# Kernel optimization log

Hardware: AMD Instinct MI355X
Metric: run time of the kernel (lower is better)

## Reference

```python
import jax, jax.numpy as jnp
import numpy as np

C, N, H = 1024, 64, 16
B, T = 4, 1024
DECAY_LORA, AAA_LORA, MV_LORA, GATE_LORA = 64, 64, 32, 128
EPS_GN = 0.00064


def setup_inputs() -> dict:
    key = jax.random.key(0)
    ks = iter(jax.random.split(key, 32))
    nrm = lambda shape, s=0.02: jax.random.normal(next(ks), shape, jnp.float32) * s
    uni = lambda shape: jax.random.uniform(next(ks), shape, jnp.float32)
    inp = {
        'x': jax.random.normal(next(ks), (B, T, C), jnp.float32),
        'x_r': uni((1, 1, C)), 'x_w': uni((1, 1, C)), 'x_k': uni((1, 1, C)),
        'x_v': uni((1, 1, C)), 'x_a': uni((1, 1, C)), 'x_g': uni((1, 1, C)),
        'w0': nrm((1, 1, C), 0.5), 'w1': nrm((C, DECAY_LORA)), 'w2': nrm((DECAY_LORA, C)),
        'a0': nrm((1, 1, C), 0.5), 'a1': nrm((C, AAA_LORA)), 'a2': nrm((AAA_LORA, C)),
        'v0': nrm((1, 1, C), 0.5), 'v1': nrm((C, MV_LORA)), 'v2': nrm((MV_LORA, C)),
        'g1': nrm((C, GATE_LORA)), 'g2': nrm((GATE_LORA, C)),
        'k_k': uni((1, 1, C)), 'k_a': uni((1, 1, C)), 'r_k': nrm((H, N), 0.1),
        'Wr': nrm((C, C)), 'Wk': nrm((C, C)), 'Wv': nrm((C, C)), 'Wo': nrm((C, C)),
        'ln_gamma': jnp.ones((C,), jnp.float32), 'ln_beta': jnp.zeros((C,), jnp.float32),
    }
    return inp


def rwkv7_op(r, w, k, v, a, b):
    # r,w,k,v,a,b: [B,T,C]; state S: [B,H,N,N] (rows=value dim, cols=key dim)
    Bb, Tt, Cc = r.shape
    to_t = lambda z: z.reshape(Bb, Tt, H, N).transpose(1, 0, 2, 3)  # [T,B,H,N]
    r_, k_, v_, a_, b_ = map(to_t, (r, k, v, a, b))
    w_ = jnp.exp(-jnp.exp(to_t(w)))  # decay in (0,1)
    def step(S, inp):
        rt, wt, kt, vt, at, bt = inp
        sa = jnp.einsum('bhij,bhj->bhi', S, at)                 # S @ a
        S = S * wt[:, :, None, :] + sa[..., None] * bt[:, :, None, :] \
            + vt[..., None] * kt[:, :, None, :]
        out = jnp.einsum('bhij,bhj->bhi', S, rt)
        return S, out
    S0 = jnp.zeros((Bb, H, N, N), r.dtype)
    _, outs = jax.lax.scan(step, S0, (r_, w_, k_, v_, a_, b_))
    return outs.transpose(1, 0, 2, 3).reshape(Bb, Tt, Cc)


def reference(x, x_r, x_w, x_k, x_v, x_a, x_g, w0, w1, w2, a0, a1, a2,
              v0, v1, v2, g1, g2, k_k, k_a, r_k, Wr, Wk, Wv, Wo,
              ln_gamma, ln_beta):
    Bb, Tt, Cc = x.shape
    # token shift
    xx = jnp.pad(x, ((0, 0), (1, 0), (0, 0)))[:, :-1] - x
    xr = x + xx * x_r; xw = x + xx * x_w; xk = x + xx * x_k
    xv = x + xx * x_v; xa = x + xx * x_a; xg = x + xx * x_g
    r = xr @ Wr
    w = -jax.nn.softplus(-(w0 + jnp.tanh(xw @ w1) @ w2)) - 0.5
    k = xk @ Wk
    v = xv @ Wv
    v_first = v  # first-layer case (v_first=None)
    a = jax.nn.sigmoid(a0 + xa @ a1 @ a2)
    g = jax.nn.sigmoid(xg @ g1) @ g2
    kk = k * k_k
    kkh = kk.reshape(Bb, Tt, H, N)
    kk = (kkh / jnp.maximum(jnp.linalg.norm(kkh, axis=-1, keepdims=True), 1e-12)).reshape(Bb, Tt, Cc)
    k = k * (1 + (a - 1) * k_a)
    o = rwkv7_op(r, w, k, v, -kk, kk * a)
    # group norm over H groups of N channels
    y = o.reshape(Bb * Tt, H, N)
    mu = jnp.mean(y, axis=-1, keepdims=True)
    var = jnp.var(y, axis=-1, keepdims=True)
    y = ((y - mu) * jax.lax.rsqrt(var + EPS_GN)).reshape(Bb, Tt, Cc) * ln_gamma + ln_beta
    rh = r.reshape(Bb, Tt, H, N)
    kh = k.reshape(Bb, Tt, H, N)
    vh = v.reshape(Bb, Tt, H, N)
    rwkv = jnp.sum(rh * kh * r_k, axis=-1, keepdims=True) * vh
    y = y + rwkv.reshape(Bb, Tt, Cc)
    out = (y * g) @ Wo
    return out, v_first
```

## Files before the change

### kernel.cpp

```cpp
#include <hip/hip_runtime.h>
#include <hip/hip_bf16.h>
#include <math.h>

#define BB 4
#define TT 1024
#define CCH 1024
#define HH 16
#define NNd 64
#define PAD 65
#define RS 72
#define LBS 68

typedef short bf16x8 __attribute__((ext_vector_type(8)));
typedef float f32x4 __attribute__((ext_vector_type(4)));

__device__ __forceinline__ unsigned short f2bf(float f) {
  __hip_bfloat16 h = __float2bfloat16(f);
  return __builtin_bit_cast(unsigned short, h);
}
__device__ __forceinline__ float bf2f(unsigned short u) {
  unsigned int x = (unsigned int)u << 16;
  return __builtin_bit_cast(float, x);
}
__device__ __forceinline__ float sigmoidf_(float x) {
  return __builtin_amdgcn_rcpf(1.0f + __expf(-x));
}
__device__ __forceinline__ float ftanh_(float x) {
  return 1.0f - 2.0f * __builtin_amdgcn_rcpf(__expf(2.0f * x) + 1.0f);
}

__device__ __forceinline__ void gl2lds16(const unsigned short* g, unsigned short* l) {
  __builtin_amdgcn_global_load_lds(
      (const __attribute__((address_space(1))) unsigned int*)g,
      (__attribute__((address_space(3))) unsigned int*)l, 16, 0, 0);
}

__device__ __forceinline__ void transpose_tile(
    const float* __restrict__ in, unsigned short* __restrict__ out,
    int R, int Cc, int r0, int c0, unsigned short (*tile)[68], int t)
{
  const int rr = t >> 4;
  const int cc = (t & 15) * 4;
#pragma unroll
  for (int p = 0; p < 4; ++p) {
    int row = p * 16 + rr;
    float4 v = *(const float4*)(in + (size_t)(r0 + row) * Cc + c0 + cc);
    tile[row][cc]     = f2bf(v.x);
    tile[row][cc + 1] = f2bf(v.y);
    tile[row][cc + 2] = f2bf(v.z);
    tile[row][cc + 3] = f2bf(v.w);
  }
  __syncthreads();
#pragma unroll
  for (int p = 0; p < 4; ++p) {
    int row = p * 16 + rr;
    ushort4 o;
    o.x = tile[cc][row];
    o.y = tile[cc + 1][row];
    o.z = tile[cc + 2][row];
    o.w = tile[cc + 3][row];
    *(ushort4*)(out + (size_t)(c0 + row) * R + r0 + cc) = o;
  }
}

__global__ __launch_bounds__(256) void prep_kernel(
    const float* __restrict__ x,
    const float* __restrict__ cr, const float* __restrict__ cw,
    const float* __restrict__ ck, const float* __restrict__ cv,
    const float* __restrict__ ca, const float* __restrict__ cg,
    unsigned short* __restrict__ xr, unsigned short* __restrict__ xw,
    unsigned short* __restrict__ xk, unsigned short* __restrict__ xv,
    unsigned short* __restrict__ xa, unsigned short* __restrict__ xg,
    const float* __restrict__ W0, const float* __restrict__ W1,
    const float* __restrict__ W2, const float* __restrict__ W3,
    unsigned short* __restrict__ T0, unsigned short* __restrict__ T1,
    unsigned short* __restrict__ T2, unsigned short* __restrict__ T3,
    const float* __restrict__ w1, const float* __restrict__ w2,
    const float* __restrict__ a1, const float* __restrict__ a2,
    const float* __restrict__ g1, const float* __restrict__ g2,
    unsigned short* __restrict__ w1T, unsigned short* __restrict__ w2T,
    unsigned short* __restrict__ a1T, unsigned short* __restrict__ a2T,
    unsigned short* __restrict__ g1T, unsigned short* __restrict__ g2T)
{
  __shared__ unsigned short tile[64][68];
  const int blk = blockIdx.x;
  const int tid = threadIdx.x;
  if (blk < 4096) {
    const size_t idx = ((size_t)blk * 256 + tid) * 4;
    const int c = (int)(idx & 1023);
    const int t = (int)((idx >> 10) & 1023);
    float4 xc = *(const float4*)(x + idx);
    float4 xp = make_float4(0.f, 0.f, 0.f, 0.f);
    if (t > 0) xp = *(const float4*)(x + idx - 1024);
    float4 dx = make_float4(xp.x - xc.x, xp.y - xc.y, xp.z - xc.z, xp.w - xc.w);
    auto st = [&](unsigned short* dst, const float* coef) {
      float4 w = *(const float4*)(coef + c);
      ushort4 o;
      o.x = f2bf(fmaf(dx.x, w.x, xc.x));
      o.y = f2bf(fmaf(dx.y, w.y, xc.y));
      o.z = f2bf(fmaf(dx.z, w.z, xc.z));
      o.w = f2bf(fmaf(dx.w, w.w, xc.w));
      *(ushort4*)(dst + idx) = o;
    };
    st(xr, cr); st(xw, cw); st(xk, ck); st(xv, cv); st(xa, ca); st(xg, cg);
  } else if (blk < 5120) {
    const int j = blk - 4096;
    const int z = j >> 8, rem = j & 255;
    const int ty = rem >> 4, tx = rem & 15;
    const float* src = (z == 0) ? W0 : (z == 1) ? W1 : (z == 2) ? W2 : W3;
    unsigned short* dst = (z == 0) ? T0 : (z == 1) ? T1 : (z == 2) ? T2 : T3;
    transpose_tile(src, dst, 1024, 1024, tx * 64, ty * 64, tile, tid);
  } else {
    const int i = blk - 5120;
    const float* src; unsigned short* dst; int R, C, rt, ct;
    if (i < 16)      { src = w1; dst = w1T; R = 1024; C = 64;   rt = i;      ct = 0; }
    else if (i < 32) { src = w2; dst = w2T; R = 64;   C = 1024; rt = 0;      ct = i - 16; }
    else if (i < 48) { src = a1; dst = a1T; R = 1024; C = 64;   rt = i - 32; ct = 0; }
    else if (i < 64) { src = a2; dst = a2T; R = 64;   C = 1024; rt = 0;      ct = i - 48; }
    else if (i < 96) { int k = i - 64; src = g1; dst = g1T; R = 1024; C = 128; rt = k >> 1; ct = k & 1; }
    else             { int k = i - 96; src = g2; dst = g2T; R = 128; C = 1024; rt = k & 1;  ct = k >> 1; }
    transpose_tile(src, dst, R, C, rt * 64, ct * 64, tile, tid);
  }
}

__global__ __launch_bounds__(256) void gemm_stage1_kernel(
    const unsigned short* __restrict__ xrB, const unsigned short* __restrict__ xkB,
    const unsigned short* __restrict__ xvB,
    const unsigned short* __restrict__ WrT, const unsigned short* __restrict__ WkT,
    const unsigned short* __restrict__ WvT,
    unsigned short* __restrict__ r_btc, unsigned short* __restrict__ k_btc,
    float* __restrict__ v_btc,
    const unsigned short* __restrict__ xwB, const unsigned short* __restrict__ xaB,
    const unsigned short* __restrict__ xgB,
    const unsigned short* __restrict__ w1T, const unsigned short* __restrict__ a1T,
    const unsigned short* __restrict__ g1T,
    unsigned short* __restrict__ hwB, unsigned short* __restrict__ haB,
    unsigned short* __restrict__ hgB)
{
  constexpr int K = 1024, SK = 32;
  __shared__ __align__(16) unsigned short As[128 * SK];
  __shared__ __align__(16) unsigned short Bs[128 * SK];
  const int blk = blockIdx.x;
  const int tid = threadIdx.x;
  const int wv = tid >> 6, lane = tid & 63;
  const int fr = lane & 15, q = lane >> 4;
  const int arow = tid >> 2;
  const int akc = (tid & 3) * 8;

  if (blk < 768) {
    const int z = blk >> 8, rem = blk & 255;
    const int m0 = (rem & 31) * 128;
    const int n0 = (rem >> 5) * 128;
    const unsigned short* A = (z == 0) ? xrB : (z == 1) ? xkB : xvB;
    const unsigned short* BT = (z == 0) ? WrT : (z == 1) ? WkT : WvT;
    const int wave_m = wv >> 1, wave_n = wv & 1;

    f32x4 acc[4][4];
#pragma unroll
    for (int i = 0; i < 4; i++)
#pragma unroll
      for (int j = 0; j < 4; j++) acc[i][j] = (f32x4){0.f, 0.f, 0.f, 0.f};

    for (int k0 = 0; k0 < K; k0 += 32) {
#pragma unroll
      for (int i = 0; i < 2; ++i)
        gl2lds16(A + (size_t)(m0 + arow + i * 64) * K + k0 + akc, As + i * 2048 + wv * 512);
#pragma unroll
      for (int i = 0; i < 2; ++i)
        gl2lds16(BT + (size_t)(n0 + arow + i * 64) * K + k0 + akc, Bs + i * 2048 + wv * 512);
      __syncthreads();
      bf16x8 af[4], bfv[4];
#pragma unroll
      for (int i = 0; i < 4; i++)
        af[i] = *(const bf16x8*)(&As[(wave_m * 64 + i * 16 + fr) * SK + q * 8]);
#pragma unroll
      for (int j = 0; j < 4; j++)
        bfv[j] = *(const bf16x8*)(&Bs[(wave_n * 64 + j * 16 + fr) * SK + q * 8]);
#pragma unroll
      for (int i = 0; i < 4; i++)
#pragma unroll
        for (int j = 0; j < 4; j++)
          acc[i][j] = __builtin_amdgcn_mfma_f32_16x16x32_bf16(af[i], bfv[j], acc[i][j], 0, 0, 0);
      __syncthreads();
    }
#pragma unroll
    for (int i = 0; i < 4; i++)
#pragma unroll
      for (int j = 0; j < 4; j++) {
        const int mb = m0 + wave_m * 64 + i * 16 + q * 4;
        const int n = n0 + wave_n * 64 + j * 16 + fr;
#pragma unroll
        for (int r = 0; r < 4; r++) {
          if (z == 0)      r_btc[(size_t)(mb + r) * 1024 + n] = f2bf(acc[i][j][r]);
          else if (z == 1) k_btc[(size_t)(mb + r) * 1024 + n] = f2bf(acc[i][j][r]);
          else             v_btc[(size_t)(mb + r) * 1024 + n] = acc[i][j][r];
        }
      }
  } else {
    const int j2 = blk - 768;
    const int y = j2 >> 5;
    const int m0 = (j2 & 31) * 128;
    const unsigned short* A  = (y == 0) ? xwB : (y == 1) ? xaB : xgB;
    const unsigned short* BT = (y == 0) ? w1T : (y == 1) ? a1T : (g1T + (size_t)(y - 2) * 64 * K);
    unsigned short* outb = (y == 0) ? hwB : (y == 1) ? haB : hgB;
    const int Nout = (y < 2) ? 64 : 128;
    const int ncol0 = (y < 2) ? 0 : (y - 2) * 64;

    f32x4 acc[2][4];
#pragma unroll
    for (int i = 0; i < 2; i++)
#pragma unroll
      for (int j = 0; j < 4; j++) acc[i][j] = (f32x4){0.f, 0.f, 0.f, 0.f};

    for (int k0 = 0; k0 < K; k0 += 32) {
#pragma unroll
      for (int i = 0; i < 2; ++i)
        gl2lds16(A + (size_t)(m0 + arow + i * 64) * K + k0 + akc, As + i * 2048 + wv * 512);
      gl2lds16(BT + (size_t)arow * K + k0 + akc, Bs + wv * 512);
      __syncthreads();
      bf16x8 af[2], bfv[4];
#pragma unroll
      for (int i = 0; i < 2; i++)
        af[i] = *(const bf16x8*)(&As[(wv * 32 + i * 16 + fr) * SK + q * 8]);
#pragma unroll
      for (int j = 0; j < 4; j++)
        bfv[j] = *(const bf16x8*)(&Bs[(j * 16 + fr) * SK + q * 8]);
#pragma unroll
      for (int i = 0; i < 2; i++)
#pragma unroll
        for (int j = 0; j < 4; j++)
          acc[i][j] = __builtin_amdgcn_mfma_f32_16x16x32_bf16(af[i], bfv[j], acc[i][j], 0, 0, 0);
      __syncthreads();
    }
#pragma unroll
    for (int i = 0; i < 2; i++)
#pragma unroll
      for (int j = 0; j < 4; j++) {
        const int mb = m0 + wv * 32 + i * 16 + q * 4;
        const int n = ncol0 + j * 16 + fr;
#pragma unroll
        for (int r = 0; r < 4; r++) {
          float val = acc[i][j][r];
          if (y == 0) val = ftanh_(val);
          else if (y >= 2) val = sigmoidf_(val);
          outb[(size_t)(mb + r) * Nout + n] = f2bf(val);
        }
      }
  }
}

__global__ __launch_bounds__(256) void lora2_kernel(
    const unsigned short* __restrict__ hwB, const unsigned short* __restrict__ haB,
    const unsigned short* __restrict__ hgB,
    const unsigned short* __restrict__ w2T, const unsigned short* __restrict__ a2T,
    const unsigned short* __restrict__ g2T,
    unsigned short* __restrict__ wraw, unsigned short* __restrict__ araw,
    unsigned short* __restrict__ gfB)
{
  constexpr int N = 1024, SK = 32;
  __shared__ __align__(16) unsigned short As[128 * SK];
  __shared__ __align__(16) unsigned short Bs[128 * SK];
  const int z = blockIdx.z;
  const unsigned short* A = (z == 0) ? hwB : (z == 1) ? haB : hgB;
  const unsigned short* BT = (z == 0) ? w2T : (z == 1) ? a2T : g2T;
  unsigned short* out = (z == 0) ? wraw : (z == 1) ? araw : gfB;
  const int K = (z == 2) ? 128 : 64;

  const int tid = threadIdx.x;
  const int wv = tid >> 6, lane = tid & 63;
  const int fr = lane & 15, q = lane >> 4;
  const int wave_m = wv >> 1, wave_n = wv & 1;
  const int m0 = blockIdx.x * 128;
  const int n0 = blockIdx.y * 128;

  f32x4 acc[4][4];
#pragma unroll
  for (int i = 0; i < 4; i++)
#pragma unroll
    for (int j = 0; j < 4; j++) acc[i][j] = (f32x4){0.f, 0.f, 0.f, 0.f};

  const int arow = tid >> 2;
  const int akc = (tid & 3) * 8;

  for (int k0 = 0; k0 < K; k0 += 32) {
#pragma unroll
    for (int i = 0; i < 2; ++i)
      gl2lds16(A + (size_t)(m0 + arow + i * 64) * K + k0 + akc, As + i * 2048 + wv * 512);
#pragma unroll
    for (int i = 0; i < 2; ++i)
      gl2lds16(BT + (size_t)(n0 + arow + i * 64) * K + k0 + akc, Bs + i * 2048 + wv * 512);
    __syncthreads();
    bf16x8 af[4], bfv[4];
#pragma unroll
    for (int i = 0; i < 4; i++)
      af[i] = *(const bf16x8*)(&As[(wave_m * 64 + i * 16 + fr) * SK + q * 8]);
#pragma unroll
    for (int j = 0; j < 4; j++)
      bfv[j] = *(const bf16x8*)(&Bs[(wave_n * 64 + j * 16 + fr) * SK + q * 8]);
#pragma unroll
    for (int i = 0; i < 4; i++)
#pragma unroll
      for (int j = 0; j < 4; j++)
        acc[i][j] = __builtin_amdgcn_mfma_f32_16x16x32_bf16(af[i], bfv[j], acc[i][j], 0, 0, 0);
    __syncthreads();
  }
#pragma unroll
  for (int i = 0; i < 4; i++)
#pragma unroll
    for (int j = 0; j < 4; j++) {
      const int mb = m0 + wave_m * 64 + i * 16 + q * 4;
      const int n = n0 + wave_n * 64 + j * 16 + fr;
#pragma unroll
      for (int r = 0; r < 4; r++)
        out[(size_t)(mb + r) * N + n] = f2bf(acc[i][j][r]);
    }
}

__global__ __launch_bounds__(256) void gemm_out_kernel(
    const unsigned short* __restrict__ A,
    const unsigned short* __restrict__ BT,
    float* __restrict__ out)
{
  constexpr int K = 1024, N = 1024, SK = 32;
  __shared__ __align__(16) unsigned short As[128 * SK];
  __shared__ __align__(16) unsigned short Bs[128 * SK];
  const int tid = threadIdx.x;
  const int wv = tid >> 6, lane = tid & 63;
  const int fr = lane & 15, q = lane >> 4;
  const int wave_m = wv >> 1, wave_n = wv & 1;
  const int m0 = blockIdx.x * 128;
  const int n0 = blockIdx.y * 128;

  f32x4 acc[4][4];
#pragma unroll
  for (int i = 0; i < 4; i++)
#pragma unroll
    for (int j = 0; j < 4; j++) acc[i][j] = (f32x4){0.f, 0.f, 0.f, 0.f};

  const int arow = tid >> 2;
  const int akc = (tid & 3) * 8;

  for (int k0 = 0; k0 < K; k0 += 32) {
#pragma unroll
    for (int i = 0; i < 2; ++i)
      gl2lds16(A + (size_t)(m0 + arow + i * 64) * K + k0 + akc, As + i * 2048 + wv * 512);
#pragma unroll
    for (int i = 0; i < 2; ++i)
      gl2lds16(BT + (size_t)(n0 + arow + i * 64) * K + k0 + akc, Bs + i * 2048 + wv * 512);
    __syncthreads();
    bf16x8 af[4], bfv[4];
#pragma unroll
    for (int i = 0; i < 4; i++)
      af[i] = *(const bf16x8*)(&As[(wave_m * 64 + i * 16 + fr) * SK + q * 8]);
#pragma unroll
    for (int j = 0; j < 4; j++)
      bfv[j] = *(const bf16x8*)(&Bs[(wave_n * 64 + j * 16 + fr) * SK + q * 8]);
#pragma unroll
    for (int i = 0; i < 4; i++)
#pragma unroll
      for (int j = 0; j < 4; j++)
        acc[i][j] = __builtin_amdgcn_mfma_f32_16x16x32_bf16(af[i], bfv[j], acc[i][j], 0, 0, 0);
    __syncthreads();
  }
#pragma unroll
  for (int i = 0; i < 4; i++)
#pragma unroll
    for (int j = 0; j < 4; j++) {
      const int mb = m0 + wave_m * 64 + i * 16 + q * 4;
      const int n = n0 + wave_n * 64 + j * 16 + fr;
#pragma unroll
      for (int r = 0; r < 4; r++)
        out[(size_t)(mb + r) * N + n] = acc[i][j][r];
    }
}

__global__ __launch_bounds__(256, 2) void chunk_ops_kernel(
    const unsigned short* __restrict__ r_btc, const unsigned short* __restrict__ k_btc,
    const float* __restrict__ v_btc, const unsigned short* __restrict__ wraw,
    const unsigned short* __restrict__ araw,
    const float* __restrict__ w0, const float* __restrict__ a0,
    const float* __restrict__ k_k, const float* __restrict__ k_a,
    const float* __restrict__ r_k,
    unsigned short* __restrict__ McG, unsigned short* __restrict__ NcG,
    unsigned short* __restrict__ PcG, unsigned short* __restrict__ OlG,
    unsigned short* __restrict__ DkG, float* __restrict__ s3G)
{
  extern __shared__ char smraw[];
  unsigned short* AHb  = (unsigned short*)smraw;
  unsigned short* RHb  = AHb + 64 * RS;
  unsigned short* BPb  = RHb + 64 * RS;
  unsigned short* KPb  = BPb + 64 * RS;
  unsigned short* BPTb = KPb + 64 * RS;
  unsigned short* KPTb = BPTb + 64 * RS;
  unsigned short* VSTb = KPTb + 64 * RS;
  unsigned short* LBb  = VSTb + 64 * RS;
  float* GLs = (float*)(LBb + 64 * LBS);
  float* SS  = GLs + 64;
  unsigned short* XTb = AHb;
  unsigned short* LKb = BPb;
  unsigned short* QTb = BPb;
  unsigned short* DBb = KPb;

  const int inst = blockIdx.x;
  const int bh = inst >> 4, c = inst & 15;
  const int b = bh >> 4, h = bh & 15;
  const int tid = threadIdx.x;
  const int lane = tid & 63;
  const int wv = tid >> 6;
  const int jl = lane;
  const int ch = h * 64 + jl;
  const size_t base = ((size_t)(b * 1024 + c * 64) * 1024) + ch;

  const float p_w0 = w0[ch], p_a0 = a0[ch];
  const float p_kk = k_k[ch], p_ka = k_a[ch], p_rk = r_k[ch];
  const float EM = 0.60653065971263342f;

  unsigned short wr_u[16], kv_u[16], rv_u[16], ar_u[16];
  float vv_u[16];
#pragma unroll
  for (int u = 0; u < 16; ++u) {
    const size_t gi = base + (size_t)(16 * wv + u) * 1024;
    wr_u[u] = wraw[gi];
    kv_u[u] = k_btc[gi];
    rv_u[u] = r_btc[gi];
    ar_u[u] = araw[gi];
    vv_u[u] = v_btc[gi];
  }

  float lwv[16];
  {
    float run = 0.f;
#pragma unroll
    for (int u = 0; u < 16; ++u) {
      run += -EM * sigmoidf_(p_w0 + bf2f(wr_u[u]));
      lwv[u] = run;
    }
    SS[wv * 64 + jl] = run;
  }
  __syncthreads();
  const float s0 = SS[0 * 64 + jl], s1 = SS[1 * 64 + jl];
  const float s2 = SS[2 * 64 + jl], s3s = SS[3 * 64 + jl];
  const float goff = (wv > 0 ? s0 : 0.f) + (wv > 1 ? s1 : 0.f) + (wv > 2 ? s2 : 0.f);
  const float gl = s0 + s1 + s2 + s3s;
  if (wv == 0) GLs[jl] = gl;

  float s3v[16];
  {
    const float e_gl = __expf(gl);
#pragma unroll
    for (int u = 0; u < 16; ++u) {
      const int t = 16 * wv + u;
      const float pre = goff + (u ? lwv[u - 1] : 0.f);
      const float cur = goff + lwv[u];
      const float kv = bf2f(kv_u[u]), rv = bf2f(rv_u[u]);
      const float vv = vv_u[u];
      const float av = sigmoidf_(p_a0 + bf2f(ar_u[u]));
      const float kkx = kv * p_kk;
      float ssq = kkx * kkx;
#pragma unroll
      for (int m = 1; m < 64; m <<= 1) ssq += __shfl_xor(ssq, m);
      const float scale = __builtin_amdgcn_rsqf(fmaxf(ssq, 1e-24f));
      const float kkn = kkx * scale;
      const float bb = kkn * av;
      const float kmod = kv * (1.0f + (av - 1.0f) * p_ka);
      float s3 = rv * kmod * p_rk;
#pragma unroll
      for (int m = 1; m < 64; m <<= 1) s3 += __shfl_xor(s3, m);
      s3v[u] = s3;
      const float e_prev = __expf(pre);
      const float e_gu   = __expf(cur);
      const float em     = __expf(-cur);
      const float egl    = e_gl * em;
      AHb[t * RS + jl] = f2bf(-kkn * e_prev);
      BPb[t * RS + jl] = f2bf(bb * em);
      KPb[t * RS + jl] = f2bf(kmod * em);
      BPTb[jl * RS + t] = f2bf(bb * egl);
      KPTb[jl * RS + t] = f2bf(kmod * egl);
      RHb[t * RS + jl] = f2bf(rv * e_gu);
      VSTb[jl * RS + t] = f2bf(vv);
    }
    if (jl == 0) {
      float* sp = s3G + (bh << 10) + (c << 6) + 16 * wv;
#pragma unroll
      for (int k2 = 0; k2 < 4; ++k2)
        *(float4*)(sp + 4 * k2) = make_float4(s3v[4 * k2], s3v[4 * k2 + 1],
                                              s3v[4 * k2 + 2], s3v[4 * k2 + 3]);
    }
  }
  __syncthreads();

  const int fr = lane & 15, q = lane >> 4;
  const int i0 = wv * 16;

  {
    f32x4 aLB[4], aLK[4], aDB[4], aDK[4];
#pragma unroll
    for (int j = 0; j < 4; ++j) {
      aLB[j] = (f32x4){0.f, 0.f, 0.f, 0.f}; aLK[j] = (f32x4){0.f, 0.f, 0.f, 0.f};
      aDB[j] = (f32x4){0.f, 0.f, 0.f, 0.f}; aDK[j] = (f32x4){0.f, 0.f, 0.f, 0.f};
    }
#pragma unroll
    for (int ks = 0; ks < 2; ++ks) {
      const int ko = ks * 32 + q * 8;
      bf16x8 fA = *(const bf16x8*)(AHb + (i0 + fr) * RS + ko);
      bf16x8 fR = *(const bf16x8*)(RHb + (i0 + fr) * RS + ko);
#pragma unroll
      for (int j = 0; j < 4; ++j) {
        bf16x8 fB = *(const bf16x8*)(BPb + (j * 16 + fr) * RS + ko);
        bf16x8 fK = *(const bf16x8*)(KPb + (j * 16 + fr) * RS + ko);
        aLB[j] = __builtin_amdgcn_mfma_f32_16x16x32_bf16(fA, fB, aLB[j], 0, 0, 0);
        aLK[j] = __builtin_amdgcn_mfma_f32_16x16x32_bf16(fA, fK, aLK[j], 0, 0, 0);
        aDB[j] = __builtin_amdgcn_mfma_f32_16x16x32_bf16(fR, fB, aDB[j], 0, 0, 0);
        aDK[j] = __builtin_amdgcn_mfma_f32_16x16x32_bf16(fR, fK, aDK[j], 0, 0, 0);
      }
    }
    __syncthreads();
#pragma unroll
    for (int j = 0; j < 4; ++j) {
      const int s = j * 16 + fr;
#pragma unroll
      for (int r = 0; r < 4; ++r) {
        const int t = i0 + q * 4 + r;
        LBb[t * LBS + s] = f2bf((s < t) ? aLB[j][r] : 0.f);
        LKb[t * RS + s] = f2bf((s < t) ? aLK[j][r] : 0.f);
        DBb[t * RS + s] = f2bf((s <= t) ? aDB[j][r] : 0.f);
        DkG[(size_t)inst * 4096 + t * 64 + s] = f2bf((s <= t) ? aDK[j][r] : 0.f);
      }
    }
  }
  __syncthreads();

  {
    f32x4 wacc[4];
#pragma unroll
    for (int j = 0; j < 4; ++j) wacc[j] = (f32x4){0.f, 0.f, 0.f, 0.f};
#pragma unroll
    for (int ks = 0; ks < 2; ++ks) {
      const int ko = ks * 32 + q * 8;
      bf16x8 fL = *(const bf16x8*)(LKb + (i0 + fr) * RS + ko);
#pragma unroll
      for (int j = 0; j < 4; ++j) {
        bf16x8 fV = *(const bf16x8*)(VSTb + (j * 16 + fr) * RS + ko);
        wacc[j] = __builtin_amdgcn_mfma_f32_16x16x32_bf16(fL, fV, wacc[j], 0, 0, 0);
      }
    }
#pragma unroll
    for (int j = 0; j < 4; ++j)
#pragma unroll
      for (int r = 0; r < 4; ++r)
        LKb[(i0 + q * 4 + r) * RS + j * 16 + fr] = f2bf(wacc[j][r]);
  }
  __syncthreads();

  bf16x8 fDK0, fDK1;
  {
    const unsigned short* dkp = DkG + (size_t)inst * 4096 + (i0 + fr) * 64 + q * 8;
    fDK0 = *(const bf16x8*)(dkp);
    fDK1 = *(const bf16x8*)(dkp + 32);
  }

  if (wv < 2) {
    const int jc = lane;
    unsigned short* Sb = (wv == 0) ? AHb : LKb;
    unsigned short* Tb = (wv == 0) ? XTb : QTb;
    float x[64];
#pragma unroll
    for (int t = 0; t < 64; ++t) x[t] = bf2f(Sb[t * RS + jc]);
#pragma unroll
    for (int z2 = 0; z2 < 8; ++z2)
      *(bf16x8*)(Tb + jc * RS + z2 * 8) = (bf16x8){0, 0, 0, 0, 0, 0, 0, 0};

    const int jf = jc & 15, tjm = jc >> 4;

#pragma unroll
    for (int I = 0; I < 4; ++I) {
      if (I > 0) {
        f32x4 cU[4];
#pragma unroll
        for (int tj = 0; tj < 4; ++tj) cU[tj] = (f32x4){0.f, 0.f, 0.f, 0.f};
#pragma unroll
        for (int kw = 0; kw < 2; ++kw) {
          if (kw * 32 < 16 * I) {
            const int ko = kw * 32 + q * 8;
            bf16x8 fL;
            *(ushort4*)&fL = *(const ushort4*)(LBb + (16 * I + fr) * LBS + ko);
            *((ushort4*)&fL + 1) = *(const ushort4*)(LBb + (16 * I + fr) * LBS + ko + 4);
#pragma unroll
            for (int tj = 0; tj < 4; ++tj) {
              bf16x8 fX = *(const bf16x8*)(Tb + (tj * 16 + fr) * RS + ko);
              cU[tj] = __builtin_amdgcn_mfma_f32_16x16x32_bf16(fL, fX, cU[tj], 0, 0, 0);
            }
          }
        }
#pragma unroll
        for (int qq = 0; qq < 4; ++qq) {
          const int saddr = (qq * 16 + jf) * 4;
#pragma unroll
          for (int r = 0; r < 4; ++r) {
            int g0 = __builtin_amdgcn_ds_bpermute(saddr, __builtin_bit_cast(int, cU[0][r]));
            int g1 = __builtin_amdgcn_ds_bpermute(saddr, __builtin_bit_cast(int, cU[1][r]));
            int g2 = __builtin_amdgcn_ds_bpermute(saddr, __builtin_bit_cast(int, cU[2][r]));
            int g3 = __builtin_amdgcn_ds_bpermute(saddr, __builtin_bit_cast(int, cU[3][r]));
            int gs = (tjm == 0) ? g0 : (tjm == 1) ? g1 : (tjm == 2) ? g2 : g3;
            x[16 * I + qq * 4 + r] += __builtin_bit_cast(float, gs);
          }
        }
      }
#pragma unroll
      for (int u = 1; u < 16; ++u) {
        const unsigned short* lr = LBb + (16 * I + u) * LBS + 16 * I;
        float acc0 = 0.f, acc1 = 0.f;
#pragma unroll
        for (int s = 0; s + 2 <= u; s += 2) {
          acc0 = fmaf(bf2f(lr[s]), x[16 * I + s], acc0);
          acc1 = fmaf(bf2f(lr[s + 1]), x[16 * I + s + 1], acc1);
        }
        if (u & 1) acc0 = fmaf(bf2f(lr[u - 1]), x[16 * I + u - 1], acc0);
        x[16 * I + u] += acc0 + acc1;
      }
#pragma unroll
      for (int t2 = 0; t2 < 16; t2 += 2) {
        unsigned int pk = (unsigned int)f2bf(x[16 * I + t2])
                        | ((unsigned int)f2bf(x[16 * I + t2 + 1]) << 16);
        *(unsigned int*)(Tb + jc * RS + 16 * I + t2) = pk;
      }
    }
  }
  __syncthreads();

  {
    f32x4 mA[4], nA[4], pA[4], oA[4];
#pragma unroll
    for (int j = 0; j < 4; ++j) {
      mA[j] = (f32x4){0.f, 0.f, 0.f, 0.f}; nA[j] = (f32x4){0.f, 0.f, 0.f, 0.f};
      pA[j] = (f32x4){0.f, 0.f, 0.f, 0.f}; oA[j] = (f32x4){0.f, 0.f, 0.f, 0.f};
    }
#pragma unroll
    for (int ks = 0; ks < 2; ++ks) {
      const int ko = ks * 32 + q * 8;
      bf16x8 fBT = *(const bf16x8*)(BPTb + (i0 + fr) * RS + ko);
      bf16x8 fKT = *(const bf16x8*)(KPTb + (i0 + fr) * RS + ko);
      bf16x8 fDB = *(const bf16x8*)(DBb + (i0 + fr) * RS + ko);
      bf16x8 fDK = ks ? fDK1 : fDK0;
#pragma unroll
      for (int j = 0; j < 4; ++j) {
        bf16x8 fXT = *(const bf16x8*)(XTb + (j * 16 + fr) * RS + ko);
        bf16x8 fQT = *(const bf16x8*)(QTb + (j * 16 + fr) * RS + ko);
        bf16x8 fVT = *(const bf16x8*)(VSTb + (j * 16 + fr) * RS + ko);
        mA[j] = __builtin_amdgcn_mfma_f32_16x16x32_bf16(fBT, fXT, mA[j], 0, 0, 0);
        nA[j] = __builtin_amdgcn_mfma_f32_16x16x32_bf16(fBT, fQT, nA[j], 0, 0, 0);
        nA[j] = __builtin_amdgcn_mfma_f32_16x16x32_bf16(fKT, fVT, nA[j], 0, 0, 0);
        pA[j] = __builtin_amdgcn_mfma_f32_16x16x32_bf16(fDB, fXT, pA[j], 0, 0, 0);
        oA[j] = __builtin_amdgcn_mfma_f32_16x16x32_bf16(fDB, fQT, oA[j], 0, 0, 0);
        oA[j] = __builtin_amdgcn_mfma_f32_16x16x32_bf16(fDK, fVT, oA[j], 0, 0, 0);
      }
    }
    const size_t ob = (size_t)inst * 4096;
    float eg[4];
#pragma unroll
    for (int r = 0; r < 4; ++r) eg[r] = __expf(GLs[i0 + q * 4 + r]);
#pragma unroll
    for (int j = 0; j < 4; ++j) {
      const int col = j * 16 + fr;
#pragma unroll
      for (int r = 0; r < 4; ++r) {
        const int row = i0 + q * 4 + r;
        const size_t oi = ob + (size_t)row * 64 + col;
        McG[oi] = f2bf(mA[j][r] + (row == col ? eg[r] : 0.f));
        NcG[oi] = f2bf(nA[j][r]);
        PcG[oi] = f2bf(pA[j][r] + bf2f(RHb[row * RS + col]));
        OlG[oi] = f2bf(oA[j][r]);
      }
    }
  }
}

__global__ __launch_bounds__(256) void chunk_scan_kernel(
    const unsigned short* __restrict__ McG, const unsigned short* __restrict__ NcG,
    unsigned short* __restrict__ Sch)
{
  __shared__ float ST[64 * PAD];
  __shared__ float MB[64 * PAD];
  const int bh = blockIdx.x;
  const int tid = threadIdx.x;
  const int it = tid >> 4, jt = tid & 15;

#pragma unroll
  for (int q = 0; q < 16; ++q) {
    int idx = q * 256 + tid;
    ST[(idx >> 6) * PAD + (idx & 63)] = 0.f;
  }
  __syncthreads();

  for (int c = 0; c < 16; ++c) {
    const size_t ob = ((((size_t)bh << 4) + c) << 12);
#pragma unroll
    for (int q = 0; q < 4; ++q) {
      int idx = q * 1024 + tid * 4;
      int row = idx >> 6, col = idx & 63;
      ushort4 sv;
      sv.x = f2bf(ST[row * PAD + col]);     sv.y = f2bf(ST[row * PAD + col + 1]);
      sv.z = f2bf(ST[row * PAD + col + 2]); sv.w = f2bf(ST[row * PAD + col + 3]);
      *(ushort4*)(Sch + ob + idx) = sv;
      ushort4 mv = *(const ushort4*)(McG + ob + idx);
      MB[row * PAD + col] = bf2f(mv.x);     MB[row * PAD + col + 1] = bf2f(mv.y);
      MB[row * PAD + col + 2] = bf2f(mv.z); MB[row * PAD + col + 3] = bf2f(mv.w);
    }
    __syncthreads();
    float acc[4][4];
#pragma unroll
    for (int u = 0; u < 4; ++u) {
      ushort4 n4 = *(const ushort4*)(NcG + ob + (size_t)(4 * it + u) * 64 + 4 * jt);
      acc[u][0] = bf2f(n4.x); acc[u][1] = bf2f(n4.y);
      acc[u][2] = bf2f(n4.z); acc[u][3] = bf2f(n4.w);
    }
#pragma unroll 4
    for (int pp = 0; pp < 64; ++pp) {
      float mv[4], sv[4];
#pragma unroll
      for (int u = 0; u < 4; ++u) mv[u] = MB[(4 * it + u) * PAD + pp];
#pragma unroll
      for (int v = 0; v < 4; ++v) sv[v] = ST[pp * PAD + 4 * jt + v];
#pragma unroll
      for (int u = 0; u < 4; ++u)
#pragma unroll
        for (int v = 0; v < 4; ++v) acc[u][v] = fmaf(mv[u], sv[v], acc[u][v]);
    }
    __syncthreads();
#pragma unroll
    for (int u = 0; u < 4; ++u)
#pragma unroll
      for (int v = 0; v < 4; ++v) ST[(4 * it + u) * PAD + 4 * jt + v] = acc[u][v];
    __syncthreads();
  }
}

__global__ __launch_bounds__(256) void chunk_outgn_kernel(
    const unsigned short* __restrict__ PcG, const unsigned short* __restrict__ OlG,
    const unsigned short* __restrict__ Sch, const float* __restrict__ s3G,
    const float* __restrict__ v_btc, const unsigned short* __restrict__ g_f,
    const float* __restrict__ gamma, const float* __restrict__ beta,
    unsigned short* __restrict__ yg)
{
  __shared__ float ST[64 * PAD];
  __shared__ float PB[64 * PAD];
  const int inst = blockIdx.x;
  const int bh = inst >> 4, c = inst & 15;
  const int b = bh >> 4, h = bh & 15;
  const int tid = threadIdx.x;
  const int tt = tid >> 4, jt = tid & 15;
  const size_t ob = (size_t)inst << 12;

#pragma unroll
  for (int q = 0; q < 4; ++q) {
    int idx = q * 1024 + tid * 4;
    int row = idx >> 6, col = idx & 63;
    ushort4 sv = *(const ushort4*)(Sch + ob + idx);
    ST[row * PAD + col] = bf2f(sv.x);     ST[row * PAD + col + 1] = bf2f(sv.y);
    ST[row * PAD + col + 2] = bf2f(sv.z); ST[row * PAD + col + 3] = bf2f(sv.w);
    ushort4 pv = *(const ushort4*)(PcG + ob + idx);
    PB[row * PAD + col] = bf2f(pv.x);     PB[row * PAD + col + 1] = bf2f(pv.y);
    PB[row * PAD + col + 2] = bf2f(pv.z); PB[row * PAD + col + 3] = bf2f(pv.w);
  }
  __syncthreads();

  float acc[4][4];
#pragma unroll
  for (int u = 0; u < 4; ++u) {
    ushort4 o4 = *(const ushort4*)(OlG + ob + (size_t)(4 * tt + u) * 64 + 4 * jt);
    acc[u][0] = bf2f(o4.x); acc[u][1] = bf2f(o4.y);
    acc[u][2] = bf2f(o4.z); acc[u][3] = bf2f(o4.w);
  }
#pragma unroll 4
  for (int pp = 0; pp < 64; ++pp) {
    float pv[4], sv[4];
#pragma unroll
    for (int u = 0; u < 4; ++u) pv[u] = PB[(4 * tt + u) * PAD + pp];
#pragma unroll
    for (int v = 0; v < 4; ++v) sv[v] = ST[pp * PAD + 4 * jt + v];
#pragma unroll
    for (int u = 0; u < 4; ++u)
#pragma unroll
      for (int v = 0; v < 4; ++v) acc[u][v] = fmaf(pv[u], sv[v], acc[u][v]);
  }

  const int colb = h * 64 + 4 * jt;
  float4 ga4 = *(const float4*)(gamma + colb);
  float4 be4 = *(const float4*)(beta + colb);

#pragma unroll
  for (int u = 0; u < 4; ++u) {
    float sum1 = acc[u][0] + acc[u][1] + acc[u][2] + acc[u][3];
    float sum2 = acc[u][0] * acc[u][0] + acc[u][1] * acc[u][1]
               + acc[u][2] * acc[u][2] + acc[u][3] * acc[u][3];
#pragma unroll
    for (int m = 1; m < 16; m <<= 1) {
      sum1 += __shfl_xor(sum1, m);
      sum2 += __shfl_xor(sum2, m);
    }
    const float mean = sum1 * (1.0f / 64.0f);
    const float var = sum2 * (1.0f / 64.0f) - mean * mean;
    const float rstd = __builtin_amdgcn_rsqf(var + 0.00064f);
    const int tok = c * 64 + 4 * tt + u;
    const float s3 = s3G[(bh << 10) + tok];
    const size_t gaddr = ((size_t)(b * 1024 + tok) * 1024) + colb;
    float4 v4 = *(const float4*)(v_btc + gaddr);
    ushort4 g4b = *(const ushort4*)(g_f + gaddr);
    ushort4 ov;
    ov.x = f2bf(((acc[u][0] - mean) * rstd * ga4.x + be4.x + s3 * v4.x) * bf2f(g4b.x));
    ov.y = f2bf(((acc[u][1] - mean) * rstd * ga4.y + be4.y + s3 * v4.y) * bf2f(g4b.y));
    ov.z = f2bf(((acc[u][2] - mean) * rstd * ga4.z + be4.z + s3 * v4.z) * bf2f(g4b.z));
    ov.w = f2bf(((acc[u][3] - mean) * rstd * ga4.w + be4.w + s3 * v4.w) * bf2f(g4b.w));
    *(ushort4*)(yg + gaddr) = ov;
  }
}

extern "C" void kernel_launch(void* const* d_in, const int* in_sizes, int n_in,
                              void* d_out, int out_size, void* d_ws, size_t ws_size,
                              hipStream_t stream)
{
  (void)in_sizes; (void)n_in; (void)out_size;
  const float* x    = (const float*)d_in[0];
  const float* x_r  = (const float*)d_in[1];
  const float* x_w  = (const float*)d_in[2];
  const float* x_k  = (const float*)d_in[3];
  const float* x_v  = (const float*)d_in[4];
  const float* x_a  = (const float*)d_in[5];
  const float* x_g  = (const float*)d_in[6];
  const float* w0   = (const float*)d_in[7];
  const float* w1   = (const float*)d_in[8];
  const float* w2   = (const float*)d_in[9];
  const float* a0   = (const float*)d_in[10];
  const float* a1   = (const float*)d_in[11];
  const float* a2   = (const float*)d_in[12];
  const float* g1   = (const float*)d_in[16];
  const float* g2   = (const float*)d_in[17];
  const float* k_k  = (const float*)d_in[18];
  const float* k_a  = (const float*)d_in[19];
  const float* r_k  = (const float*)d_in[20];
  const float* Wr   = (const float*)d_in[21];
  const float* Wk   = (const float*)d_in[22];
  const float* Wv   = (const float*)d_in[23];
  const float* Wo   = (const float*)d_in[24];
  const float* ln_g = (const float*)d_in[25];
  const float* ln_b = (const float*)d_in[26];

  float* outp = (float*)d_out;
  float* vfirst = outp + (size_t)BB * TT * CCH;

  char* ws = (char*)d_ws;
  size_t off = 0;
  auto alloc = [&](size_t bytes) -> char* {
    char* p = ws + off;
    off += (bytes + 255) & ~(size_t)255;
    return p;
  };

  unsigned short* WrT = (unsigned short*)alloc(2097152);
  unsigned short* WkT = (unsigned short*)alloc(2097152);
  unsigned short* WvT = (unsigned short*)alloc(2097152);
  unsigned short* WoT = (unsigned short*)alloc(2097152);
  unsigned short* w1T = (unsigned short*)alloc(131072);
  unsigned short* w2T = (unsigned short*)alloc(131072);
  unsigned short* a1T = (unsigned short*)alloc(131072);
  unsigned short* a2T = (unsigned short*)alloc(131072);
  unsigned short* g1T = (unsigned short*)alloc(262144);
  unsigned short* g2T = (unsigned short*)alloc(262144);
  unsigned short* xrB = (unsigned short*)alloc(8388608);
  unsigned short* xwB = (unsigned short*)alloc(8388608);
  unsigned short* xkB = (unsigned short*)alloc(8388608);
  unsigned short* xvB = (unsigned short*)alloc(8388608);
  unsigned short* xaB = (unsigned short*)alloc(8388608);
  unsigned short* xgB = (unsigned short*)alloc(8388608);
  unsigned short* r_btc = (unsigned short*)alloc(8388608);
  unsigned short* k_btc = (unsigned short*)alloc(8388608);
  unsigned short* wraw  = (unsigned short*)alloc(8388608);
  unsigned short* araw  = (unsigned short*)alloc(8388608);
  unsigned short* gfB = (unsigned short*)alloc(8388608);
  unsigned short* OlG = (unsigned short*)alloc(8388608);
  unsigned short* DkG = (unsigned short*)alloc(8388608);
  float* s3G   = (float*)alloc(262144);
  unsigned short* hwB = (unsigned short*)alloc(524288);
  unsigned short* haB = (unsigned short*)alloc(524288);
  unsigned short* hgB = (unsigned short*)alloc(1048576);
  unsigned short* ygB = (unsigned short*)alloc(8388608);

  unsigned short* McG = xrB;
  unsigned short* NcG = xkB;
  unsigned short* PcG = xaB;
  unsigned short* Sch = k_btc;

  if (off > ws_size) return;

  dim3 blk(256);

  prep_kernel<<<5248, blk, 0, stream>>>(
      x, x_r, x_w, x_k, x_v, x_a, x_g,
      xrB, xwB, xkB, xvB, xaB, xgB,
      Wr, Wk, Wv, Wo, WrT, WkT, WvT, WoT,
      w1, w2, a1, a2, g1, g2, w1T, w2T, a1T, a2T, g1T, g2T);

  gemm_stage1_kernel<<<896, blk, 0, stream>>>(
      xrB, xkB, xvB, WrT, WkT, WvT, r_btc, k_btc, vfirst,
      xwB, xaB, xgB, w1T, a1T, g1T, hwB, haB, hgB);

  lora2_kernel<<<dim3(32, 8, 3), blk, 0, stream>>>(
      hwB, haB, hgB, w2T, a2T, g2T, wraw, araw, gfB);

  constexpr int CHUNK_LDS = 7 * 64 * RS * 2 + 64 * LBS * 2 + 64 * 4 + 4 * 64 * 4;
  hipFuncSetAttribute((const void*)chunk_ops_kernel,
                      hipFuncAttributeMaxDynamicSharedMemorySize, CHUNK_LDS);
  chunk_ops_kernel<<<1024, blk, CHUNK_LDS, stream>>>(
      r_btc, k_btc, vfirst, wraw, araw, w0, a0, k_k, k_a, r_k,
      McG, NcG, PcG, OlG, DkG, s3G);

  chunk_scan_kernel<<<64, blk, 0, stream>>>(McG, NcG, Sch);

  chunk_outgn_kernel<<<1024, blk, 0, stream>>>(PcG, OlG, Sch, s3G, vfirst, gfB,
                                               ln_g, ln_b, ygB);

  gemm_out_kernel<<<dim3(32, 8), blk, 0, stream>>>(ygB, WoT, outp);
}
```

Before: 352.5 us.

## Use bf16 MFMA with hi/lo state split in chunk scan kernel

Rewrites the sequential inter-chunk state recurrence to run on MFMA matrix instructions instead of scalar FMA loops. The fp32 state is kept in registers and split into bf16 high and low parts so precision stays close to fp32. The transition matrix is loaded straight from global memory into fragments, which removes the shared-memory staging buffer. The first chunk is peeled so that no matmul runs against a zero state. The cost is twice the MFMA work for the hi/lo split and transposed shared-memory writes.

```diff
diff --git a/kernel.cpp b/kernel.cpp
--- a/kernel.cpp
+++ b/kernel.cpp
@@ -679,59 +679,63 @@
     const unsigned short* __restrict__ McG, const unsigned short* __restrict__ NcG,
     unsigned short* __restrict__ Sch)
 {
-  __shared__ float ST[64 * PAD];
-  __shared__ float MB[64 * PAD];
+  __shared__ __align__(16) unsigned short STh[64 * RS];
+  __shared__ __align__(16) unsigned short STl[64 * RS];
   const int bh = blockIdx.x;
   const int tid = threadIdx.x;
-  const int it = tid >> 4, jt = tid & 15;
-
-#pragma unroll
-  for (int q = 0; q < 16; ++q) {
-    int idx = q * 256 + tid;
-    ST[(idx >> 6) * PAD + (idx & 63)] = 0.f;
-  }
-  __syncthreads();
-
-  for (int c = 0; c < 16; ++c) {
-    const size_t ob = ((((size_t)bh << 4) + c) << 12);
-#pragma unroll
-    for (int q = 0; q < 4; ++q) {
-      int idx = q * 1024 + tid * 4;
-      int row = idx >> 6, col = idx & 63;
-      ushort4 sv;
-      sv.x = f2bf(ST[row * PAD + col]);     sv.y = f2bf(ST[row * PAD + col + 1]);
-      sv.z = f2bf(ST[row * PAD + col + 2]); sv.w = f2bf(ST[row * PAD + col + 3]);
-      *(ushort4*)(Sch + ob + idx) = sv;
-      ushort4 mv = *(const ushort4*)(McG + ob + idx);
-      MB[row * PAD + col] = bf2f(mv.x);     MB[row * PAD + col + 1] = bf2f(mv.y);
-      MB[row * PAD + col + 2] = bf2f(mv.z); MB[row * PAD + col + 3] = bf2f(mv.w);
-    }
+  const int wv = tid >> 6, lane = tid & 63;
+  const int fr = lane & 15, q = lane >> 4;
+
+  f32x4 acc[4];
+
+  {
+    const size_t ob = ((size_t)bh << 4) << 12;
+#pragma unroll
+    for (int j = 0; j < 4; ++j) {
+      const int col = j * 16 + fr;
+#pragma unroll
+      for (int r = 0; r < 4; ++r) {
+        const int row = wv * 16 + q * 4 + r;
+        Sch[ob + (size_t)row * 64 + col] = 0;
+        acc[j][r] = bf2f(NcG[ob + (size_t)row * 64 + col]);
+      }
+    }
+  }
+
+  for (int c = 1; c < 16; ++c) {
+    const size_t ob = ((((size_t)bh << 4) + (size_t)c) << 12);
     __syncthreads();
-    float acc[4][4];
-#pragma unroll
-    for (int u = 0; u < 4; ++u) {
-      ushort4 n4 = *(const ushort4*)(NcG + ob + (size_t)(4 * it + u) * 64 + 4 * jt);
-      acc[u][0] = bf2f(n4.x); acc[u][1] = bf2f(n4.y);
-      acc[u][2] = bf2f(n4.z); acc[u][3] = bf2f(n4.w);
-    }
-#pragma unroll 4
-    for (int pp = 0; pp < 64; ++pp) {
-      float mv[4], sv[4];
-#pragma unroll
-      for (int u = 0; u < 4; ++u) mv[u] = MB[(4 * it + u) * PAD + pp];
-#pragma unroll
-      for (int v = 0; v < 4; ++v) sv[v] = ST[pp * PAD + 4 * jt + v];
-#pragma unroll
-      for (int u = 0; u < 4; ++u)
-#pragma unroll
-        for (int v = 0; v < 4; ++v) acc[u][v] = fmaf(mv[u], sv[v], acc[u][v]);
+#pragma unroll
+    for (int j = 0; j < 4; ++j) {
+      const int col = j * 16 + fr;
+#pragma unroll
+      for (int r = 0; r < 4; ++r) {
+        const int row = wv * 16 + q * 4 + r;
+        const float v = acc[j][r];
+        const unsigned short hi = f2bf(v);
+        STh[col * RS + row] = hi;
+        STl[col * RS + row] = f2bf(v - bf2f(hi));
+        Sch[ob + (size_t)row * 64 + col] = hi;
+      }
     }
     __syncthreads();
-#pragma unroll
-    for (int u = 0; u < 4; ++u)
-#pragma unroll
-      for (int v = 0; v < 4; ++v) ST[(4 * it + u) * PAD + 4 * jt + v] = acc[u][v];
-    __syncthreads();
+    const bf16x8 fA0 = *(const bf16x8*)(McG + ob + (size_t)(wv * 16 + fr) * 64 + q * 8);
+    const bf16x8 fA1 = *(const bf16x8*)(McG + ob + (size_t)(wv * 16 + fr) * 64 + 32 + q * 8);
+#pragma unroll
+    for (int j = 0; j < 4; ++j) {
+      const int col = j * 16 + fr;
+#pragma unroll
+      for (int r = 0; r < 4; ++r)
+        acc[j][r] = bf2f(NcG[ob + (size_t)(wv * 16 + q * 4 + r) * 64 + col]);
+      const bf16x8 h0 = *(const bf16x8*)(STh + (j * 16 + fr) * RS + q * 8);
+      const bf16x8 h1 = *(const bf16x8*)(STh + (j * 16 + fr) * RS + 32 + q * 8);
+      const bf16x8 l0 = *(const bf16x8*)(STl + (j * 16 + fr) * RS + q * 8);
+      const bf16x8 l1 = *(const bf16x8*)(STl + (j * 16 + fr) * RS + 32 + q * 8);
+      acc[j] = __builtin_amdgcn_mfma_f32_16x16x32_bf16(fA0, h0, acc[j], 0, 0, 0);
+      acc[j] = __builtin_amdgcn_mfma_f32_16x16x32_bf16(fA1, h1, acc[j], 0, 0, 0);
+      acc[j] = __builtin_amdgcn_mfma_f32_16x16x32_bf16(fA0, l0, acc[j], 0, 0, 0);
+      acc[j] = __builtin_amdgcn_mfma_f32_16x16x32_bf16(fA1, l1, acc[j], 0, 0, 0);
+    }
   }
 }
 
```

Result: faster. 317.6 us (-9.9%).
